# Optimization experiments

Measured on AMD Instinct MI355X. Metric: run time of the kernel, lower is better.

The kernel has to match this reference:

```python
import jax, jax.numpy as jnp
import numpy as np

B, C, H, W = 16, 384, 56, 56
NH, WS, SS = 12, 7, 3          # num_heads, window_size, shift_size
MLP = 4 * C
N = WS * WS                     # tokens per window (49)
nHW = H // WS                   # windows per side (8)
nW = nHW * nHW                  # windows per image (64)
HD = C // NH                    # head dim (32)
EPS = 1e-5


def _ln(x, g, b):
    mu = jnp.mean(x, axis=-1, keepdims=True)
    var = jnp.mean(jnp.square(x - mu), axis=-1, keepdims=True)
    return (x - mu) * jax.lax.rsqrt(var + EPS) * g + b


def _attn_mask():
    # static shifted-window mask, computed once with numpy (constants)
    img = np.zeros((H, W))
    sl = (slice(0, -WS), slice(-WS, -SS), slice(-SS, None))
    cnt = 0
    for hs in sl:
        for ws_ in sl:
            img[hs, ws_] = cnt
            cnt += 1
    mw = img.reshape(nHW, WS, nHW, WS).transpose(0, 2, 1, 3).reshape(-1, N)
    d = mw[:, None, :] - mw[:, :, None]          # (nW, N, N)
    return jnp.asarray(np.where(d != 0, -100.0, 0.0), jnp.float32)

_MASK = _attn_mask()


def setup_inputs() -> dict:
    key = jax.random.key(0)
    ks = jax.random.split(key, 6)
    rn = lambda k, s: jax.random.normal(k, s, jnp.float32) * 0.02
    return {
        "x": jax.random.normal(ks[0], (B, C, H, W), jnp.float32),
        "norm1_g": jnp.ones((C,), jnp.float32),
        "norm1_b": jnp.zeros((C,), jnp.float32),
        "qkv_w": rn(ks[1], (C, 3 * C)),
        "qkv_b": jnp.zeros((3 * C,), jnp.float32),
        "proj_w": rn(ks[2], (C, C)),
        "proj_b": jnp.zeros((C,), jnp.float32),
        "norm2_g": jnp.ones((C,), jnp.float32),
        "norm2_b": jnp.zeros((C,), jnp.float32),
        "fc1_w": rn(ks[3], (C, MLP)),
        "fc1_b": jnp.zeros((MLP,), jnp.float32),
        "fc2_w": rn(ks[4], (MLP, C)),
        "fc2_b": jnp.zeros((C,), jnp.float32),
    }


def reference(x, norm1_g, norm1_b, qkv_w, qkv_b, proj_w, proj_b,
              norm2_g, norm2_b, fc1_w, fc1_b, fc2_w, fc2_b):
    shortcut = x                                   # (B, C, H, W)
    xh = jnp.transpose(x, (0, 2, 3, 1))            # (B, H, W, C)
    xh = _ln(xh, norm1_g, norm1_b)
    # H, W divisible by WS -> padding is a no-op; shifted window path
    xs = jnp.roll(xh, (-SS, -SS), axis=(1, 2))
    # window partition -> (B*nW, N, C)
    xw = xs.reshape(B, nHW, WS, nHW, WS, C).transpose(0, 1, 3, 2, 4, 5)
    xw = xw.reshape(-1, N, C)
    # attention
    qkv = (xw @ qkv_w + qkv_b).reshape(-1, N, 3, NH, HD).transpose(2, 0, 3, 1, 4)
    q, k, v = qkv[0] * HD ** -0.5, qkv[1], qkv[2]  # (B*nW, NH, N, HD)
    attn = jnp.einsum('whnd,whmd->whnm', q, k)     # (B*nW, NH, N, N)
    attn = attn.reshape(B, nW, NH, N, N) + _MASK[None, :, None]
    attn = jax.nn.softmax(attn, axis=-1).reshape(-1, NH, N, N)
    out = jnp.einsum('whnm,whmd->whnd', attn, v)   # (B*nW, NH, N, HD)
    out = out.transpose(0, 2, 1, 3).reshape(-1, N, C)
    out = out @ proj_w + proj_b
    # window reverse -> (B, H, W, C), un-shift
    xs = out.reshape(B, nHW, nHW, WS, WS, C).transpose(0, 1, 3, 2, 4, 5)
    xs = xs.reshape(B, H, W, C)
    xh = jnp.roll(xs, (SS, SS), axis=(1, 2))
    x2 = shortcut + jnp.transpose(xh, (0, 3, 1, 2))
    # MLP residual (in BHWC)
    xh2 = jnp.transpose(x2, (0, 2, 3, 1))
    h = jax.nn.gelu(_ln(xh2, norm2_g, norm2_b) @ fc1_w + fc1_b,
                    approximate=False) @ fc2_w + fc2_b
    xh2 = xh2 + h
    return jnp.transpose(xh2, (0, 3, 1, 2))
```

## Files before the change

kernel.cpp:

```cpp
#include <hip/hip_runtime.h>
#include <hip/hip_bf16.h>
#include <math.h>
#include <stdint.h>

#define C_ 384
#define TOKENS 50176

typedef __bf16 bf16;
typedef __bf16 bf16x8 __attribute__((ext_vector_type(8)));
typedef __bf16 bf16x4 __attribute__((ext_vector_type(4)));
typedef float  f32x4  __attribute__((ext_vector_type(4)));

__device__ __forceinline__ float b2f(bf16 x) { return (float)x; }
__device__ __forceinline__ bf16  f2b(float x) { return (bf16)x; }

__device__ __forceinline__ float fast_gelu(float v) {
    float u2 = v * fmaf(v * v, 0.07135481f, 1.5957691f);
    return v / (1.0f + __expf(-u2));
}

__device__ __forceinline__ void gld_lds16(const bf16* g, bf16* l) {
    __builtin_amdgcn_global_load_lds(
        (const __attribute__((address_space(1))) void*)g,
        (__attribute__((address_space(3))) void*)l, 16, 0, 0);
}

__global__ void wtrans_kernel(const float* __restrict__ in, bf16* __restrict__ out,
                              int K, int N) {
    int idx = blockIdx.x * 256 + threadIdx.x;
    if (idx >= K * N) return;
    int n = idx / K, k = idx % K;
    out[idx] = f2b(in[(size_t)k * N + n]);
}

__global__ __launch_bounds__(256) void ln1_gather_kernel(
    const float* __restrict__ x, const float* __restrict__ g,
    const float* __restrict__ bt, bf16* __restrict__ xw) {
    int wave = threadIdx.x >> 6, lane = threadIdx.x & 63;
    int T = blockIdx.x * 4 + wave;
    int wi = T / 49, n = T % 49;
    int b = wi >> 6, w64 = wi & 63;
    int bh = w64 >> 3, bw = w64 & 7;
    int hs = bh * 7 + n / 7 + 3; if (hs >= 56) hs -= 56;
    int wsd = bw * 7 + n % 7 + 3; if (wsd >= 56) wsd -= 56;
    const float* xp = x + (size_t)b * C_ * 3136 + hs * 56 + wsd;
    float v[6];
    #pragma unroll
    for (int k = 0; k < 6; k++) v[k] = xp[(size_t)(lane + k * 64) * 3136];
    float s = v[0] + v[1] + v[2] + v[3] + v[4] + v[5];
    #pragma unroll
    for (int m = 32; m; m >>= 1) s += __shfl_xor(s, m);
    float mu = s * (1.0f / 384.0f);
    float s2 = 0.f;
    #pragma unroll
    for (int k = 0; k < 6; k++) { float d = v[k] - mu; s2 += d * d; }
    #pragma unroll
    for (int m = 32; m; m >>= 1) s2 += __shfl_xor(s2, m);
    float rstd = rsqrtf(s2 * (1.0f / 384.0f) + 1e-5f);
    bf16* op = xw + (size_t)T * 384;
    #pragma unroll
    for (int k = 0; k < 6; k++) {
        int c = lane + k * 64;
        op[c] = f2b((v[k] - mu) * rstd * g[c] + bt[c]);
    }
}

enum { EPI_NONE = 0, EPI_GELU = 1, EPI_PROJ = 2, EPI_FC2 = 3 };

__device__ __forceinline__ void stage_tile(const bf16* const (&gA)[4], const bf16* const (&gB)[4],
                                           bf16* Asb, bf16* Bsb, int t, int k0) {
    #pragma unroll
    for (int p = 0; p < 4; p++) gld_lds16(gA[p] + k0, Asb + (p * 256 + t) * 8);
    #pragma unroll
    for (int p = 0; p < 4; p++) gld_lds16(gB[p] + k0, Bsb + (p * 256 + t) * 8);
}

__device__ __forceinline__ void compute_tile(const bf16* Asb, const bf16* Bsb,
                                             int aoff0, int aoff1, int boff0, int boff1,
                                             f32x4 (&acc)[4][4]) {
    bf16x8 af[2][4], bfr[2][4];
    __builtin_amdgcn_sched_barrier(0);
    #pragma unroll
    for (int i = 0; i < 4; i++) {
        af[0][i] = *(const bf16x8*)((const char*)Asb + aoff0 + i * 2048);
        af[1][i] = *(const bf16x8*)((const char*)Asb + aoff1 + i * 2048);
    }
    #pragma unroll
    for (int j = 0; j < 4; j++) {
        bfr[0][j] = *(const bf16x8*)((const char*)Bsb + boff0 + j * 2048);
        bfr[1][j] = *(const bf16x8*)((const char*)Bsb + boff1 + j * 2048);
    }
    __builtin_amdgcn_sched_barrier(0);
    __builtin_amdgcn_s_setprio(1);
    #pragma unroll
    for (int kk = 0; kk < 2; kk++)
        #pragma unroll
        for (int j = 0; j < 4; j++)
            #pragma unroll
            for (int i = 0; i < 4; i++)
                acc[j][i] = __builtin_amdgcn_mfma_f32_16x16x32_bf16(bfr[kk][j], af[kk][i], acc[j][i], 0, 0, 0);
    __builtin_amdgcn_s_setprio(0);
    __builtin_amdgcn_sched_barrier(0);
}

#define SYNC_FENCE() do { __builtin_amdgcn_sched_barrier(0); \
                          __builtin_amdgcn_s_barrier(); \
                          __builtin_amdgcn_sched_barrier(0); } while (0)

template <int EPI>
__global__ __launch_bounds__(256, 2) void gemm_kernel(
    const bf16* __restrict__ A, const bf16* __restrict__ Wt,
    const float* __restrict__ bias, bf16* __restrict__ Cout,
    int Kdim, int Ndim,
    const float* __restrict__ resx,
    const bf16* __restrict__ resb) {
    __shared__ __align__(16) bf16 As[2][128 * 64];
    __shared__ __align__(16) bf16 Bs[2][128 * 64];
    int t = threadIdx.x;

    int nwg = gridDim.x * gridDim.y;
    int bid = blockIdx.y * gridDim.x + blockIdx.x;
    int q8 = nwg >> 3, r8 = nwg & 7, xcd = bid & 7, off = bid >> 3;
    int swz = (xcd < r8 ? xcd * (q8 + 1) : r8 * (q8 + 1) + (xcd - r8) * q8) + off;
    int n0 = (swz % gridDim.x) * 128;
    int m0 = (swz / gridDim.x) * 128;

    int lane = t & 63, wave = t >> 6;
    int wr = wave >> 1, wc = wave & 1;
    int quad = lane >> 4, lm = lane & 15;
    f32x4 acc[4][4] = {};

    const bf16* gA[4]; const bf16* gB[4];
    #pragma unroll
    for (int p = 0; p < 4; p++) {
        int idx = p * 256 + t;
        int row = idx >> 3, g = idx & 7;
        int gs = g ^ (row & 7);
        gA[p] = A  + (size_t)(m0 + row) * Kdim + gs * 8;
        gB[p] = Wt + (size_t)(n0 + row) * Kdim + gs * 8;
    }

    int g0 = quad ^ (lm & 7);
    int aoff0 = ((wr * 64 + lm) * 64 + g0 * 8) * 2;
    int boff0 = ((wc * 64 + lm) * 64 + g0 * 8) * 2;
    int aoff1 = aoff0 ^ 64;
    int boff1 = boff0 ^ 64;

    int nt = Kdim >> 6;
    stage_tile(gA, gB, As[0], Bs[0], t, 0);
    stage_tile(gA, gB, As[1], Bs[1], t, 64);
    asm volatile("s_waitcnt vmcnt(8)" ::: "memory");
    SYNC_FENCE();

    for (int tk = 0; tk < nt; tk += 2) {
        compute_tile(As[0], Bs[0], aoff0, aoff1, boff0, boff1, acc);
        SYNC_FENCE();
        if (tk + 2 < nt) {
            stage_tile(gA, gB, As[0], Bs[0], t, (tk + 2) << 6);
            asm volatile("s_waitcnt vmcnt(8)" ::: "memory");
        } else {
            asm volatile("s_waitcnt vmcnt(0)" ::: "memory");
        }
        SYNC_FENCE();
        compute_tile(As[1], Bs[1], aoff0, aoff1, boff0, boff1, acc);
        if (tk + 2 < nt) {
            SYNC_FENCE();
            if (tk + 3 < nt) {
                stage_tile(gA, gB, As[1], Bs[1], t, (tk + 3) << 6);
                asm volatile("s_waitcnt vmcnt(8)" ::: "memory");
            } else {
                asm volatile("s_waitcnt vmcnt(0)" ::: "memory");
            }
            SYNC_FENCE();
        }
    }

    #pragma unroll
    for (int i = 0; i < 4; i++) {
        int m = m0 + wr * 64 + i * 16 + lm;
        size_t resbase = 0;
        if (EPI == EPI_PROJ) {
            int wi = m / 49, n_ = m % 49;
            int b = wi >> 6, w64 = wi & 63;
            int bh = w64 >> 3, bw = w64 & 7;
            int hs = bh * 7 + n_ / 7 + 3; if (hs >= 56) hs -= 56;
            int wsd = bw * 7 + n_ % 7 + 3; if (wsd >= 56) wsd -= 56;
            resbase = (size_t)b * C_ * 3136 + hs * 56 + wsd;
        }
        #pragma unroll
        for (int j = 0; j < 4; j++) {
            int nb = n0 + wc * 64 + j * 16 + quad * 4;
            f32x4 bj = *(const f32x4*)(bias + nb);
            f32x4 v;
            #pragma unroll
            for (int r = 0; r < 4; r++) v[r] = acc[j][i][r] + bj[r];
            if (EPI == EPI_GELU) {
                #pragma unroll
                for (int r = 0; r < 4; r++) v[r] = fast_gelu(v[r]);
            }
            if (EPI == EPI_PROJ) {
                #pragma unroll
                for (int r = 0; r < 4; r++) v[r] += resx[resbase + (size_t)(nb + r) * 3136];
            }
            if (EPI == EPI_FC2) {
                bf16x4 rb = *(const bf16x4*)(resb + (size_t)m * 384 + nb);
                #pragma unroll
                for (int r = 0; r < 4; r++) v[r] += b2f(rb[r]);
            }
            bf16x4 o;
            #pragma unroll
            for (int r = 0; r < 4; r++) o[r] = f2b(v[r]);
            *(bf16x4*)(Cout + (size_t)m * Ndim + nb) = o;
        }
    }
}

__global__ __launch_bounds__(64) void attn_mfma_kernel(const bf16* __restrict__ qkv,
                                                       bf16* __restrict__ aout) {
    __shared__ __align__(16) bf16 pbuf[64 * 72];
    __shared__ int reg_[64];
    int l = threadIdx.x;
    int wi = blockIdx.x / 12, h = blockIdx.x % 12;
    int i16 = l & 15, quad = l >> 4;

    {
        int tok = l < 49 ? l : 48;
        int w64 = wi & 63;
        int bh = w64 >> 3, bw = w64 & 7;
        int hh = bh * 7 + tok / 7, ww = bw * 7 + tok % 7;
        int fh = hh < 49 ? 0 : (hh < 53 ? 1 : 2);
        int fw = ww < 49 ? 0 : (ww < 53 ? 1 : 2);
        reg_[l] = fh * 3 + fw;
    }
    __syncthreads();

    const bf16* qbase = qkv + (size_t)wi * 49 * 1152 + h * 32;

    f32x4 s_[4][4] = {};
    bf16x8 af[4], bfr[4];
    #pragma unroll
    for (int mi = 0; mi < 4; mi++) {
        int m = mi * 16 + i16; if (m > 48) m = 48;
        af[mi] = *(const bf16x8*)(qbase + (size_t)m * 1152 + quad * 8);
    }
    #pragma unroll
    for (int nt = 0; nt < 4; nt++) {
        int n = nt * 16 + i16; if (n > 48) n = 48;
        bfr[nt] = *(const bf16x8*)(qbase + 384 + (size_t)n * 1152 + quad * 8);
    }
    #pragma unroll
    for (int mi = 0; mi < 4; mi++)
        #pragma unroll
        for (int nt = 0; nt < 4; nt++)
            s_[mi][nt] = __builtin_amdgcn_mfma_f32_16x16x32_bf16(af[mi], bfr[nt], s_[mi][nt], 0, 0, 0);

    int creg[4];
    #pragma unroll
    for (int nt = 0; nt < 4; nt++) {
        int c = nt * 16 + i16; if (c > 48) c = 48;
        creg[nt] = reg_[c];
    }

    const float scale = 0.17677669529663687f;
    #pragma unroll
    for (int mi = 0; mi < 4; mi++) {
        #pragma unroll
        for (int r = 0; r < 4; r++) {
            int row = mi * 16 + quad * 4 + r;
            int rreg = reg_[row];
            float v[4]; float mx = -1e30f;
            #pragma unroll
            for (int nt = 0; nt < 4; nt++) {
                int c = nt * 16 + i16;
                float x = s_[mi][nt][r] * scale;
                if (c > 48) x = -1e30f;
                else if (rreg != creg[nt]) x -= 100.0f;
                v[nt] = x; mx = fmaxf(mx, x);
            }
            #pragma unroll
            for (int m = 8; m; m >>= 1) mx = fmaxf(mx, __shfl_xor(mx, m));
            float sum = 0.f;
            #pragma unroll
            for (int nt = 0; nt < 4; nt++) { v[nt] = __expf(v[nt] - mx); sum += v[nt]; }
            #pragma unroll
            for (int m = 8; m; m >>= 1) sum += __shfl_xor(sum, m);
            float inv = 1.0f / sum;
            #pragma unroll
            for (int nt = 0; nt < 4; nt++)
                pbuf[row * 72 + nt * 16 + i16] = f2b(v[nt] * inv);
        }
    }
    __syncthreads();

    f32x4 o_[4][2] = {};
    const bf16* vbase = qkv + (size_t)wi * 49 * 1152 + 768 + h * 32;
    #pragma unroll
    for (int ks = 0; ks < 2; ks++) {
        bf16x8 pa[4];
        #pragma unroll
        for (int mi = 0; mi < 4; mi++)
            pa[mi] = *(const bf16x8*)(pbuf + (mi * 16 + i16) * 72 + ks * 32 + quad * 8);
        bf16x8 vb[2];
        #pragma unroll
        for (int nt = 0; nt < 2; nt++)
            #pragma unroll
            for (int j = 0; j < 8; j++) {
                int tok = ks * 32 + quad * 8 + j; if (tok > 48) tok = 48;
                vb[nt][j] = vbase[(size_t)tok * 1152 + nt * 16 + i16];
            }
        #pragma unroll
        for (int mi = 0; mi < 4; mi++)
            #pragma unroll
            for (int nt = 0; nt < 2; nt++)
                o_[mi][nt] = __builtin_amdgcn_mfma_f32_16x16x32_bf16(pa[mi], vb[nt], o_[mi][nt], 0, 0, 0);
    }

    bf16* obase = aout + (size_t)wi * 49 * 384 + h * 32;
    #pragma unroll
    for (int mi = 0; mi < 4; mi++)
        #pragma unroll
        for (int r = 0; r < 4; r++) {
            int row = mi * 16 + quad * 4 + r;
            if (row < 49) {
                #pragma unroll
                for (int nt = 0; nt < 2; nt++)
                    obase[(size_t)row * 384 + nt * 16 + i16] = f2b(o_[mi][nt][r]);
            }
        }
}

__global__ __launch_bounds__(256) void ln2_kernel(const bf16* __restrict__ x2,
                                                  const float* __restrict__ g,
                                                  const float* __restrict__ bt,
                                                  bf16* __restrict__ x2n) {
    int wave = threadIdx.x >> 6, lane = threadIdx.x & 63;
    int T = blockIdx.x * 4 + wave;
    const bf16* xp = x2 + (size_t)T * 384;
    float v[6];
    #pragma unroll
    for (int k = 0; k < 6; k++) v[k] = b2f(xp[lane + k * 64]);
    float s = v[0] + v[1] + v[2] + v[3] + v[4] + v[5];
    #pragma unroll
    for (int m = 32; m; m >>= 1) s += __shfl_xor(s, m);
    float mu = s * (1.0f / 384.0f);
    float s2 = 0.f;
    #pragma unroll
    for (int k = 0; k < 6; k++) { float d = v[k] - mu; s2 += d * d; }
    #pragma unroll
    for (int m = 32; m; m >>= 1) s2 += __shfl_xor(s2, m);
    float rstd = rsqrtf(s2 * (1.0f / 384.0f) + 1e-5f);
    bf16* op = x2n + (size_t)T * 384;
    #pragma unroll
    for (int k = 0; k < 6; k++) {
        int c = lane + k * 64;
        op[c] = f2b((v[k] - mu) * rstd * g[c] + bt[c]);
    }
}

__global__ __launch_bounds__(256) void untile_kernel(const bf16* __restrict__ otok,
                                                     float* __restrict__ out) {
    __shared__ float tile[56 * 65];
    int t = threadIdx.x;
    int b = blockIdx.x / 336;
    int rem = blockIdx.x % 336;
    int h = rem / 6;
    int c0 = (rem % 6) * 64;
    int hs = h + 53; if (hs >= 56) hs -= 56;
    int bh = hs / 7, th = hs % 7;
    #pragma unroll
    for (int pass = 0; pass < 14; pass++) {
        int w = pass * 4 + (t >> 6);
        int c = t & 63;
        int wsd = w + 53; if (wsd >= 56) wsd -= 56;
        int T = (b * 64 + bh * 8 + wsd / 7) * 49 + th * 7 + wsd % 7;
        tile[w * 65 + c] = b2f(otok[(size_t)T * 384 + c0 + c]);
    }
    __syncthreads();
    #pragma unroll
    for (int pass = 0; pass < 14; pass++) {
        int idx = pass * 256 + t;
        int c = idx / 56, w = idx % 56;
        out[((size_t)(b * 384 + c0 + c)) * 3136 + h * 56 + w] = tile[w * 65 + c];
    }
}

extern "C" void kernel_launch(void* const* d_in, const int* in_sizes, int n_in,
                              void* d_out, int out_size, void* d_ws, size_t ws_size,
                              hipStream_t stream) {
    (void)in_sizes; (void)n_in; (void)out_size; (void)ws_size;
    const float* x      = (const float*)d_in[0];
    const float* n1g    = (const float*)d_in[1];
    const float* n1b    = (const float*)d_in[2];
    const float* qkv_w  = (const float*)d_in[3];
    const float* qkv_b  = (const float*)d_in[4];
    const float* proj_w = (const float*)d_in[5];
    const float* proj_b = (const float*)d_in[6];
    const float* n2g    = (const float*)d_in[7];
    const float* n2b    = (const float*)d_in[8];
    const float* fc1_w  = (const float*)d_in[9];
    const float* fc1_b  = (const float*)d_in[10];
    const float* fc2_w  = (const float*)d_in[11];
    const float* fc2_b  = (const float*)d_in[12];
    float* out = (float*)d_out;
    char* ws = (char*)d_ws;

    bf16* qkv_wT = (bf16*)(ws + 0);
    bf16* proj_wT = (bf16*)(ws + 884736);
    bf16* fc1_wT = (bf16*)(ws + 1179648);
    bf16* fc2_wT = (bf16*)(ws + 2359296);
    bf16* xw   = (bf16*)(ws + 4194304);
    bf16* qkvb = (bf16*)(ws + 42729472);
    bf16* attn = (bf16*)(ws + 158334976);
    bf16* x2   = (bf16*)(ws + 4194304);
    bf16* x2n  = (bf16*)(ws + 42729472);
    bf16* h1   = (bf16*)(ws + 81264640);
    bf16* otok = (bf16*)(ws + 235405312);

    wtrans_kernel<<<(384 * 1152 + 255) / 256, 256, 0, stream>>>(qkv_w, qkv_wT, 384, 1152);
    wtrans_kernel<<<(384 * 384 + 255) / 256, 256, 0, stream>>>(proj_w, proj_wT, 384, 384);
    wtrans_kernel<<<(384 * 1536 + 255) / 256, 256, 0, stream>>>(fc1_w, fc1_wT, 384, 1536);
    wtrans_kernel<<<(1536 * 384 + 255) / 256, 256, 0, stream>>>(fc2_w, fc2_wT, 1536, 384);

    ln1_gather_kernel<<<TOKENS / 4, 256, 0, stream>>>(x, n1g, n1b, xw);

    gemm_kernel<EPI_NONE><<<dim3(9, 392), 256, 0, stream>>>(
        xw, qkv_wT, qkv_b, qkvb, 384, 1152, nullptr, nullptr);

    attn_mfma_kernel<<<12288, 64, 0, stream>>>(qkvb, attn);

    gemm_kernel<EPI_PROJ><<<dim3(3, 392), 256, 0, stream>>>(
        attn, proj_wT, proj_b, x2, 384, 384, x, nullptr);

    ln2_kernel<<<TOKENS / 4, 256, 0, stream>>>(x2, n2g, n2b, x2n);

    gemm_kernel<EPI_GELU><<<dim3(12, 392), 256, 0, stream>>>(
        x2n, fc1_wT, fc1_b, h1, 384, 1536, nullptr, nullptr);

    gemm_kernel<EPI_FC2><<<dim3(3, 392), 256, 0, stream>>>(
        h1, fc2_wT, fc2_b, otok, 1536, 384, nullptr, x2);

    untile_kernel<<<16 * 336, 256, 0, stream>>>(otok, out);
}
```

Baseline: 654.0 us.

## Add persistent weight-stationary GEMM for K=384 layers with streamed A tiles

Adds a persistent 512-thread GEMM kernel that loads a full 128x384 weight panel into LDS once. It then streams 256-row A tiles through a double buffer, with epilogues fused per tile, across 252 workgroups. The qkv, proj and fc1 GEMMs use this kernel, while fc2 keeps the old kernel because its K is 1536. The goal is to stop reloading weight tiles for every output tile and to save launch/tail overhead, at the cost of one workgroup per CU and large LDS use.

```diff
diff --git a/kernel.cpp b/kernel.cpp
--- a/kernel.cpp
+++ b/kernel.cpp
@@ -5,6 +5,7 @@
 
 #define C_ 384
 #define TOKENS 50176
+#define MTILES 196
 
 typedef __bf16 bf16;
 typedef __bf16 bf16x8 __attribute__((ext_vector_type(8)));
@@ -24,6 +25,10 @@
         (const __attribute__((address_space(1))) void*)g,
         (__attribute__((address_space(3))) void*)l, 16, 0, 0);
 }
+
+#define SYNC_FENCE() do { __builtin_amdgcn_sched_barrier(0); \
+                          __builtin_amdgcn_s_barrier(); \
+                          __builtin_amdgcn_sched_barrier(0); } while (0)
 
 __global__ void wtrans_kernel(const float* __restrict__ in, bf16* __restrict__ out,
                               int K, int N) {
@@ -67,17 +72,160 @@
 
 enum { EPI_NONE = 0, EPI_GELU = 1, EPI_PROJ = 2, EPI_FC2 = 3 };
 
-__device__ __forceinline__ void stage_tile(const bf16* const (&gA)[4], const bf16* const (&gB)[4],
-                                           bf16* Asb, bf16* Bsb, int t, int k0) {
+
+__device__ __forceinline__ void stage_A(const bf16* const (&gAs)[4], bf16* dst,
+                                        int t, int koff) {
+    #pragma unroll
+    for (int p = 0; p < 4; p++) gld_lds16(gAs[p] + koff, dst + (p * 512 + t) * 8);
+}
+
+__device__ __forceinline__ void compute_step(const bf16* Asb, const bf16* Wsb,
+                                             int abase, int wbase, int tkb,
+                                             f32x4 (&acc)[4][4]) {
+    bf16x8 af[2][4], bw[2][4];
+    __builtin_amdgcn_sched_barrier(0);
+    #pragma unroll
+    for (int i = 0; i < 4; i++) {
+        af[0][i] = *(const bf16x8*)((const char*)Asb + abase + i * 2048);
+        af[1][i] = *(const bf16x8*)((const char*)Asb + (abase ^ 64) + i * 2048);
+    }
+    #pragma unroll
+    for (int j = 0; j < 4; j++) {
+        bw[0][j] = *(const bf16x8*)((const char*)Wsb + wbase + tkb + j * 12288);
+        bw[1][j] = *(const bf16x8*)((const char*)Wsb + (wbase ^ 64) + tkb + j * 12288);
+    }
+    __builtin_amdgcn_sched_barrier(0);
+    __builtin_amdgcn_s_setprio(1);
+    #pragma unroll
+    for (int kk = 0; kk < 2; kk++)
+        #pragma unroll
+        for (int j = 0; j < 4; j++)
+            #pragma unroll
+            for (int i = 0; i < 4; i++)
+                acc[j][i] = __builtin_amdgcn_mfma_f32_16x16x32_bf16(bw[kk][j], af[kk][i], acc[j][i], 0, 0, 0);
+    __builtin_amdgcn_s_setprio(0);
+    __builtin_amdgcn_sched_barrier(0);
+}
+
+template <int EPI>
+__global__ __launch_bounds__(512, 1) void gemm_wp_kernel(
+    const bf16* __restrict__ A, const bf16* __restrict__ Wt,
+    const float* __restrict__ bias, bf16* __restrict__ Cout,
+    int Ndim, int NPANEL, int PPN,
+    const float* __restrict__ resx) {
+    __shared__ __align__(16) bf16 As[2][256 * 64];
+    __shared__ __align__(16) bf16 Ws[128 * 384];
+    int t = threadIdx.x;
+    int panel = blockIdx.x % NPANEL, pb = blockIdx.x / NPANEL;
+    int n0 = panel * 128;
+    int lo = (MTILES * pb) / PPN, hi = (MTILES * (pb + 1)) / PPN;
+    int ntile = hi - lo;
+
+    #pragma unroll
+    for (int q = 0; q < 12; q++) {
+        int idx = q * 512 + t;
+        int row = idx / 48, cg = idx % 48;
+        int sg = (cg & ~7) | ((cg & 7) ^ (row & 7));
+        gld_lds16(Wt + (size_t)(n0 + row) * 384 + sg * 8, &Ws[0] + idx * 8);
+    }
+    const bf16* gAs[4];
+    #pragma unroll
+    for (int q = 0; q < 4; q++) {
+        int idx = q * 512 + t;
+        int row = idx >> 3, g = idx & 7;
+        int gs = g ^ (row & 7);
+        gAs[q] = A + (size_t)(lo * 256 + row) * 384 + gs * 8;
+    }
+    stage_A(gAs, As[0], t, 0);
+    stage_A(gAs, As[1], t, 64);
+    int sk = 2;
+    int remaining = ntile * 6 - 2;
+    asm volatile("s_waitcnt vmcnt(4)" ::: "memory");
+    SYNC_FENCE();
+
+    int lane = t & 63, wave = t >> 6;
+    int wr = wave >> 1, wc = wave & 1;
+    int quad = lane >> 4, lm = lane & 15;
+    int g0b = (quad ^ (lm & 7)) * 16;
+    int abase = (wr * 64 + lm) * 128 + g0b;
+    int wbase = (wc * 64 + lm) * 768 + g0b;
+    f32x4 acc[4][4] = {};
+
+    int par = 0;
+    for (int lmt = 0; lmt < ntile; ++lmt) {
+        #pragma unroll
+        for (int tk = 0; tk < 6; ++tk) {
+            compute_step(As[par], Ws, abase, wbase, tk * 128, acc);
+            if (tk == 5) {
+                int m0e = (lo + lmt) * 256;
+                #pragma unroll
+                for (int i = 0; i < 4; i++) {
+                    int m = m0e + wr * 64 + i * 16 + lm;
+                    size_t resbase = 0;
+                    if (EPI == EPI_PROJ) {
+                        int wi = m / 49, n_ = m % 49;
+                        int b = wi >> 6, w64 = wi & 63;
+                        int bh = w64 >> 3, bw = w64 & 7;
+                        int hs = bh * 7 + n_ / 7 + 3; if (hs >= 56) hs -= 56;
+                        int wsd = bw * 7 + n_ % 7 + 3; if (wsd >= 56) wsd -= 56;
+                        resbase = (size_t)b * C_ * 3136 + hs * 56 + wsd;
+                    }
+                    #pragma unroll
+                    for (int j = 0; j < 4; j++) {
+                        int nb = n0 + wc * 64 + j * 16 + quad * 4;
+                        f32x4 bj = *(const f32x4*)(bias + nb);
+                        f32x4 v;
+                        #pragma unroll
+                        for (int r = 0; r < 4; r++) v[r] = acc[j][i][r] + bj[r];
+                        if (EPI == EPI_GELU) {
+                            #pragma unroll
+                            for (int r = 0; r < 4; r++) v[r] = fast_gelu(v[r]);
+                        }
+                        if (EPI == EPI_PROJ) {
+                            #pragma unroll
+                            for (int r = 0; r < 4; r++) v[r] += resx[resbase + (size_t)(nb + r) * 3136];
+                        }
+                        bf16x4 o;
+                        #pragma unroll
+                        for (int r = 0; r < 4; r++) o[r] = f2b(v[r]);
+                        *(bf16x4*)(Cout + (size_t)m * Ndim + nb) = o;
+                        #pragma unroll
+                        for (int r = 0; r < 4; r++) acc[j][i][r] = 0.f;
+                    }
+                }
+            }
+            SYNC_FENCE();
+            if (remaining > 0) {
+                stage_A(gAs, As[par], t, sk * 64);
+                remaining--;
+                if (++sk == 6) {
+                    sk = 0;
+                    #pragma unroll
+                    for (int q = 0; q < 4; q++) gAs[q] += 256 * 384;
+                }
+                if (tk == 5) asm volatile("s_waitcnt vmcnt(20)" ::: "memory");
+                else         asm volatile("s_waitcnt vmcnt(4)"  ::: "memory");
+            } else {
+                if (tk == 5) asm volatile("s_waitcnt vmcnt(16)" ::: "memory");
+                else         asm volatile("s_waitcnt vmcnt(0)"  ::: "memory");
+            }
+            SYNC_FENCE();
+            par ^= 1;
+        }
+    }
+}
+
+__device__ __forceinline__ void stage_tile4(const bf16* const (&gA)[4], const bf16* const (&gB)[4],
+                                            bf16* Asb, bf16* Bsb, int t, int k0) {
     #pragma unroll
     for (int p = 0; p < 4; p++) gld_lds16(gA[p] + k0, Asb + (p * 256 + t) * 8);
     #pragma unroll
     for (int p = 0; p < 4; p++) gld_lds16(gB[p] + k0, Bsb + (p * 256 + t) * 8);
 }
 
-__device__ __forceinline__ void compute_tile(const bf16* Asb, const bf16* Bsb,
-                                             int aoff0, int aoff1, int boff0, int boff1,
-                                             f32x4 (&acc)[4][4]) {
+__device__ __forceinline__ void compute_tile4(const bf16* Asb, const bf16* Bsb,
+                                              int aoff0, int aoff1, int boff0, int boff1,
+                                              f32x4 (&acc)[4][4]) {
     bf16x8 af[2][4], bfr[2][4];
     __builtin_amdgcn_sched_barrier(0);
     #pragma unroll
@@ -102,10 +250,6 @@
     __builtin_amdgcn_s_setprio(0);
     __builtin_amdgcn_sched_barrier(0);
 }
-
-#define SYNC_FENCE() do { __builtin_amdgcn_sched_barrier(0); \
-                          __builtin_amdgcn_s_barrier(); \
-                          __builtin_amdgcn_sched_barrier(0); } while (0)
 
 template <int EPI>
 __global__ __launch_bounds__(256, 2) void gemm_kernel(
@@ -147,26 +291,26 @@
     int boff1 = boff0 ^ 64;
 
     int nt = Kdim >> 6;
-    stage_tile(gA, gB, As[0], Bs[0], t, 0);
-    stage_tile(gA, gB, As[1], Bs[1], t, 64);
+    stage_tile4(gA, gB, As[0], Bs[0], t, 0);
+    stage_tile4(gA, gB, As[1], Bs[1], t, 64);
     asm volatile("s_waitcnt vmcnt(8)" ::: "memory");
     SYNC_FENCE();
 
     for (int tk = 0; tk < nt; tk += 2) {
-        compute_tile(As[0], Bs[0], aoff0, aoff1, boff0, boff1, acc);
+        compute_tile4(As[0], Bs[0], aoff0, aoff1, boff0, boff1, acc);
         SYNC_FENCE();
         if (tk + 2 < nt) {
-            stage_tile(gA, gB, As[0], Bs[0], t, (tk + 2) << 6);
+            stage_tile4(gA, gB, As[0], Bs[0], t, (tk + 2) << 6);
             asm volatile("s_waitcnt vmcnt(8)" ::: "memory");
         } else {
             asm volatile("s_waitcnt vmcnt(0)" ::: "memory");
         }
         SYNC_FENCE();
-        compute_tile(As[1], Bs[1], aoff0, aoff1, boff0, boff1, acc);
+        compute_tile4(As[1], Bs[1], aoff0, aoff1, boff0, boff1, acc);
         if (tk + 2 < nt) {
             SYNC_FENCE();
             if (tk + 3 < nt) {
-                stage_tile(gA, gB, As[1], Bs[1], t, (tk + 3) << 6);
+                stage_tile4(gA, gB, As[1], Bs[1], t, (tk + 3) << 6);
                 asm volatile("s_waitcnt vmcnt(8)" ::: "memory");
             } else {
                 asm volatile("s_waitcnt vmcnt(0)" ::: "memory");
@@ -178,15 +322,6 @@
     #pragma unroll
     for (int i = 0; i < 4; i++) {
         int m = m0 + wr * 64 + i * 16 + lm;
-        size_t resbase = 0;
-        if (EPI == EPI_PROJ) {
-            int wi = m / 49, n_ = m % 49;
-            int b = wi >> 6, w64 = wi & 63;
-            int bh = w64 >> 3, bw = w64 & 7;
-            int hs = bh * 7 + n_ / 7 + 3; if (hs >= 56) hs -= 56;
-            int wsd = bw * 7 + n_ % 7 + 3; if (wsd >= 56) wsd -= 56;
-            resbase = (size_t)b * C_ * 3136 + hs * 56 + wsd;
-        }
         #pragma unroll
         for (int j = 0; j < 4; j++) {
             int nb = n0 + wc * 64 + j * 16 + quad * 4;
@@ -197,10 +332,6 @@
             if (EPI == EPI_GELU) {
                 #pragma unroll
                 for (int r = 0; r < 4; r++) v[r] = fast_gelu(v[r]);
-            }
-            if (EPI == EPI_PROJ) {
-                #pragma unroll
-                for (int r = 0; r < 4; r++) v[r] += resx[resbase + (size_t)(nb + r) * 3136];
             }
             if (EPI == EPI_FC2) {
                 bf16x4 rb = *(const bf16x4*)(resb + (size_t)m * 384 + nb);
@@ -423,18 +554,18 @@
 
     ln1_gather_kernel<<<TOKENS / 4, 256, 0, stream>>>(x, n1g, n1b, xw);
 
-    gemm_kernel<EPI_NONE><<<dim3(9, 392), 256, 0, stream>>>(
-        xw, qkv_wT, qkv_b, qkvb, 384, 1152, nullptr, nullptr);
+    gemm_wp_kernel<EPI_NONE><<<252, 512, 0, stream>>>(
+        xw, qkv_wT, qkv_b, qkvb, 1152, 9, 28, nullptr);
 
     attn_mfma_kernel<<<12288, 64, 0, stream>>>(qkvb, attn);
 
-    gemm_kernel<EPI_PROJ><<<dim3(3, 392), 256, 0, stream>>>(
-        attn, proj_wT, proj_b, x2, 384, 384, x, nullptr);
+    gemm_wp_kernel<EPI_PROJ><<<252, 512, 0, stream>>>(
+        attn, proj_wT, proj_b, x2, 384, 3, 84, x);
 
     ln2_kernel<<<TOKENS / 4, 256, 0, stream>>>(x2, n2g, n2b, x2n);
 
-    gemm_kernel<EPI_GELU><<<dim3(12, 392), 256, 0, stream>>>(
-        x2n, fc1_wT, fc1_b, h1, 384, 1536, nullptr, nullptr);
+    gemm_wp_kernel<EPI_GELU><<<252, 512, 0, stream>>>(
+        x2n, fc1_wT, fc1_b, h1, 1536, 12, 21, nullptr);
 
     gemm_kernel<EPI_FC2><<<dim3(3, 392), 256, 0, stream>>>(
         h1, fc2_wT, fc2_b, otok, 1536, 384, nullptr, x2);
```

New measurement: 714.8 us. 9.3% more time.

## Enlarge GEMM tiles to 512x128 with 8 waves and interleaved LDS/MFMA

Applied to the files above, without the earlier changes.

The shared GEMM kernel moves from 128x128 tiles with 4 waves to 512x128 tiles with 8 waves. Each wave now computes a 128x64 sub-tile, which raises arithmetic intensity and cuts the number of B-tile reloads. The compute step is split into four MFMA groups, with the LDS loads for the next group issued between them and paced by explicit lgkmcnt waits. The cost is larger LDS use (160KB double-buffered), one block per CU, more accumulator registers, and fewer blocks in the grid, which could hurt occupancy and tail balance.

```diff
diff --git a/kernel.cpp b/kernel.cpp
--- a/kernel.cpp
+++ b/kernel.cpp
@@ -24,6 +24,10 @@
         (const __attribute__((address_space(1))) void*)g,
         (__attribute__((address_space(3))) void*)l, 16, 0, 0);
 }
+
+#define SYNC_FENCE() do { __builtin_amdgcn_sched_barrier(0); \
+                          __builtin_amdgcn_s_barrier(); \
+                          __builtin_amdgcn_sched_barrier(0); } while (0)
 
 __global__ void wtrans_kernel(const float* __restrict__ in, bf16* __restrict__ out,
                               int K, int N) {
@@ -67,54 +71,68 @@
 
 enum { EPI_NONE = 0, EPI_GELU = 1, EPI_PROJ = 2, EPI_FC2 = 3 };
 
-__device__ __forceinline__ void stage_tile(const bf16* const (&gA)[4], const bf16* const (&gB)[4],
+
+__device__ __forceinline__ void stage_tile(const bf16* const (&gA)[8], const bf16* const (&gB)[2],
                                            bf16* Asb, bf16* Bsb, int t, int k0) {
     #pragma unroll
-    for (int p = 0; p < 4; p++) gld_lds16(gA[p] + k0, Asb + (p * 256 + t) * 8);
-    #pragma unroll
-    for (int p = 0; p < 4; p++) gld_lds16(gB[p] + k0, Bsb + (p * 256 + t) * 8);
-}
-
-__device__ __forceinline__ void compute_tile(const bf16* Asb, const bf16* Bsb,
-                                             int aoff0, int aoff1, int boff0, int boff1,
-                                             f32x4 (&acc)[4][4]) {
-    bf16x8 af[2][4], bfr[2][4];
+    for (int p = 0; p < 8; p++) gld_lds16(gA[p] + k0, Asb + (p * 512 + t) * 8);
+    #pragma unroll
+    for (int p = 0; p < 2; p++) gld_lds16(gB[p] + k0, Bsb + (p * 512 + t) * 8);
+}
+
+#define MFMA16(ACC, BQ, AQ, IB)                                                   \
+    do {                                                                          \
+        __builtin_amdgcn_s_setprio(1);                                            \
+        _Pragma("unroll")                                                         \
+        for (int j_ = 0; j_ < 4; j_++)                                            \
+            _Pragma("unroll")                                                     \
+            for (int i_ = 0; i_ < 4; i_++)                                        \
+                ACC[(IB) + i_][j_] = __builtin_amdgcn_mfma_f32_16x16x32_bf16(     \
+                    BQ[j_], AQ[i_], ACC[(IB) + i_][j_], 0, 0, 0);                 \
+        __builtin_amdgcn_s_setprio(0);                                            \
+        __builtin_amdgcn_sched_barrier(0);                                        \
+    } while (0)
+
+__device__ __forceinline__ void compute_step(const bf16* Asb, const bf16* Bsb,
+                                             int aB, int bB, f32x4 (&acc)[8][4]) {
+    const char* Ab = (const char*)Asb;
+    const char* Bb = (const char*)Bsb;
+    bf16x8 a0[4], a1[4], b0[4], b1[4];
     __builtin_amdgcn_sched_barrier(0);
     #pragma unroll
-    for (int i = 0; i < 4; i++) {
-        af[0][i] = *(const bf16x8*)((const char*)Asb + aoff0 + i * 2048);
-        af[1][i] = *(const bf16x8*)((const char*)Asb + aoff1 + i * 2048);
-    }
-    #pragma unroll
-    for (int j = 0; j < 4; j++) {
-        bfr[0][j] = *(const bf16x8*)((const char*)Bsb + boff0 + j * 2048);
-        bfr[1][j] = *(const bf16x8*)((const char*)Bsb + boff1 + j * 2048);
-    }
+    for (int i = 0; i < 4; i++) a0[i] = *(const bf16x8*)(Ab + aB + i * 2048);
+    #pragma unroll
+    for (int j = 0; j < 4; j++) b0[j] = *(const bf16x8*)(Bb + bB + j * 2048);
+    #pragma unroll
+    for (int i = 0; i < 4; i++) a1[i] = *(const bf16x8*)(Ab + aB + (i + 4) * 2048);
+    asm volatile("s_waitcnt lgkmcnt(4)" ::: "memory");
     __builtin_amdgcn_sched_barrier(0);
-    __builtin_amdgcn_s_setprio(1);
-    #pragma unroll
-    for (int kk = 0; kk < 2; kk++)
-        #pragma unroll
-        for (int j = 0; j < 4; j++)
-            #pragma unroll
-            for (int i = 0; i < 4; i++)
-                acc[j][i] = __builtin_amdgcn_mfma_f32_16x16x32_bf16(bfr[kk][j], af[kk][i], acc[j][i], 0, 0, 0);
-    __builtin_amdgcn_s_setprio(0);
+    MFMA16(acc, b0, a0, 0);
+    #pragma unroll
+    for (int i = 0; i < 4; i++) a0[i] = *(const bf16x8*)(Ab + (aB ^ 64) + i * 2048);
+    #pragma unroll
+    for (int j = 0; j < 4; j++) b1[j] = *(const bf16x8*)(Bb + (bB ^ 64) + j * 2048);
+    asm volatile("s_waitcnt lgkmcnt(8)" ::: "memory");
     __builtin_amdgcn_sched_barrier(0);
-}
-
-#define SYNC_FENCE() do { __builtin_amdgcn_sched_barrier(0); \
-                          __builtin_amdgcn_s_barrier(); \
-                          __builtin_amdgcn_sched_barrier(0); } while (0)
+    MFMA16(acc, b0, a1, 4);
+    #pragma unroll
+    for (int i = 0; i < 4; i++) a1[i] = *(const bf16x8*)(Ab + (aB ^ 64) + (i + 4) * 2048);
+    asm volatile("s_waitcnt lgkmcnt(4)" ::: "memory");
+    __builtin_amdgcn_sched_barrier(0);
+    MFMA16(acc, b1, a0, 0);
+    asm volatile("s_waitcnt lgkmcnt(0)" ::: "memory");
+    __builtin_amdgcn_sched_barrier(0);
+    MFMA16(acc, b1, a1, 4);
+}
 
 template <int EPI>
-__global__ __launch_bounds__(256, 2) void gemm_kernel(
+__global__ __launch_bounds__(512, 1) void gemm_kernel(
     const bf16* __restrict__ A, const bf16* __restrict__ Wt,
     const float* __restrict__ bias, bf16* __restrict__ Cout,
     int Kdim, int Ndim,
     const float* __restrict__ resx,
     const bf16* __restrict__ resb) {
-    __shared__ __align__(16) bf16 As[2][128 * 64];
+    __shared__ __align__(16) bf16 As[2][512 * 64];
     __shared__ __align__(16) bf16 Bs[2][128 * 64];
     int t = threadIdx.x;
 
@@ -123,51 +141,47 @@
     int q8 = nwg >> 3, r8 = nwg & 7, xcd = bid & 7, off = bid >> 3;
     int swz = (xcd < r8 ? xcd * (q8 + 1) : r8 * (q8 + 1) + (xcd - r8) * q8) + off;
     int n0 = (swz % gridDim.x) * 128;
-    int m0 = (swz / gridDim.x) * 128;
+    int m0 = (swz / gridDim.x) * 512;
 
     int lane = t & 63, wave = t >> 6;
     int wr = wave >> 1, wc = wave & 1;
     int quad = lane >> 4, lm = lane & 15;
-    f32x4 acc[4][4] = {};
-
-    const bf16* gA[4]; const bf16* gB[4];
-    #pragma unroll
-    for (int p = 0; p < 4; p++) {
-        int idx = p * 256 + t;
+    f32x4 acc[8][4] = {};
+
+    const bf16* gA[8]; const bf16* gB[2];
+    #pragma unroll
+    for (int p = 0; p < 8; p++) {
+        int idx = p * 512 + t;
         int row = idx >> 3, g = idx & 7;
         int gs = g ^ (row & 7);
-        gA[p] = A  + (size_t)(m0 + row) * Kdim + gs * 8;
+        gA[p] = A + (size_t)(m0 + row) * Kdim + gs * 8;
+    }
+    #pragma unroll
+    for (int p = 0; p < 2; p++) {
+        int idx = p * 512 + t;
+        int row = idx >> 3, g = idx & 7;
+        int gs = g ^ (row & 7);
         gB[p] = Wt + (size_t)(n0 + row) * Kdim + gs * 8;
     }
 
-    int g0 = quad ^ (lm & 7);
-    int aoff0 = ((wr * 64 + lm) * 64 + g0 * 8) * 2;
-    int boff0 = ((wc * 64 + lm) * 64 + g0 * 8) * 2;
-    int aoff1 = aoff0 ^ 64;
-    int boff1 = boff0 ^ 64;
+    int g0b = (quad ^ (lm & 7)) * 16;
+    int aB = (wr * 128 + lm) * 128 + g0b;
+    int bB = (wc * 64 + lm) * 128 + g0b;
 
     int nt = Kdim >> 6;
     stage_tile(gA, gB, As[0], Bs[0], t, 0);
     stage_tile(gA, gB, As[1], Bs[1], t, 64);
-    asm volatile("s_waitcnt vmcnt(8)" ::: "memory");
+    asm volatile("s_waitcnt vmcnt(10)" ::: "memory");
     SYNC_FENCE();
 
-    for (int tk = 0; tk < nt; tk += 2) {
-        compute_tile(As[0], Bs[0], aoff0, aoff1, boff0, boff1, acc);
-        SYNC_FENCE();
-        if (tk + 2 < nt) {
-            stage_tile(gA, gB, As[0], Bs[0], t, (tk + 2) << 6);
-            asm volatile("s_waitcnt vmcnt(8)" ::: "memory");
-        } else {
-            asm volatile("s_waitcnt vmcnt(0)" ::: "memory");
-        }
-        SYNC_FENCE();
-        compute_tile(As[1], Bs[1], aoff0, aoff1, boff0, boff1, acc);
-        if (tk + 2 < nt) {
+    for (int tk = 0; tk < nt; ++tk) {
+        int par = tk & 1;
+        compute_step(As[par], Bs[par], aB, bB, acc);
+        if (tk + 1 < nt) {
             SYNC_FENCE();
-            if (tk + 3 < nt) {
-                stage_tile(gA, gB, As[1], Bs[1], t, (tk + 3) << 6);
-                asm volatile("s_waitcnt vmcnt(8)" ::: "memory");
+            if (tk + 2 < nt) {
+                stage_tile(gA, gB, As[par], Bs[par], t, (tk + 2) << 6);
+                asm volatile("s_waitcnt vmcnt(10)" ::: "memory");
             } else {
                 asm volatile("s_waitcnt vmcnt(0)" ::: "memory");
             }
@@ -176,8 +190,8 @@
     }
 
     #pragma unroll
-    for (int i = 0; i < 4; i++) {
-        int m = m0 + wr * 64 + i * 16 + lm;
+    for (int i = 0; i < 8; i++) {
+        int m = m0 + wr * 128 + i * 16 + lm;
         size_t resbase = 0;
         if (EPI == EPI_PROJ) {
             int wi = m / 49, n_ = m % 49;
@@ -193,7 +207,7 @@
             f32x4 bj = *(const f32x4*)(bias + nb);
             f32x4 v;
             #pragma unroll
-            for (int r = 0; r < 4; r++) v[r] = acc[j][i][r] + bj[r];
+            for (int r = 0; r < 4; r++) v[r] = acc[i][j][r] + bj[r];
             if (EPI == EPI_GELU) {
                 #pragma unroll
                 for (int r = 0; r < 4; r++) v[r] = fast_gelu(v[r]);
@@ -423,20 +437,20 @@
 
     ln1_gather_kernel<<<TOKENS / 4, 256, 0, stream>>>(x, n1g, n1b, xw);
 
-    gemm_kernel<EPI_NONE><<<dim3(9, 392), 256, 0, stream>>>(
+    gemm_kernel<EPI_NONE><<<dim3(9, 98), 512, 0, stream>>>(
         xw, qkv_wT, qkv_b, qkvb, 384, 1152, nullptr, nullptr);
 
     attn_mfma_kernel<<<12288, 64, 0, stream>>>(qkvb, attn);
 
-    gemm_kernel<EPI_PROJ><<<dim3(3, 392), 256, 0, stream>>>(
+    gemm_kernel<EPI_PROJ><<<dim3(3, 98), 512, 0, stream>>>(
         attn, proj_wT, proj_b, x2, 384, 384, x, nullptr);
 
     ln2_kernel<<<TOKENS / 4, 256, 0, stream>>>(x2, n2g, n2b, x2n);
 
-    gemm_kernel<EPI_GELU><<<dim3(12, 392), 256, 0, stream>>>(
+    gemm_kernel<EPI_GELU><<<dim3(12, 98), 512, 0, stream>>>(
         x2n, fc1_wT, fc1_b, h1, 384, 1536, nullptr, nullptr);
 
-    gemm_kernel<EPI_FC2><<<dim3(3, 392), 256, 0, stream>>>(
+    gemm_kernel<EPI_FC2><<<dim3(3, 98), 512, 0, stream>>>(
         h1, fc2_wT, fc2_b, otok, 1536, 384, nullptr, x2);
 
     untile_kernel<<<16 * 336, 256, 0, stream>>>(otok, out);
```

Result: slower. 761.9 us (+16.5%).

## Load GEMM A operand directly from global into registers, bypassing LDS

Applied to the files above, without the earlier changes.

The GEMM kernel no longer stages the A tile in shared memory. Each wave loads its A fragments straight from global memory into registers with inline global_load_dwordx4, double-buffered across even and odd k-tiles, while B is still staged through LDS with async global-to-LDS loads. This halves LDS traffic and shared memory per block, which could allow more occupancy. In exchange, global accesses per thread are less coalesced, register pressure rises from the A prefetch buffers, and the hand-counted vmcnt waits must stay exactly right.

```diff
diff --git a/kernel.cpp b/kernel.cpp
--- a/kernel.cpp
+++ b/kernel.cpp
@@ -24,6 +24,13 @@
         (const __attribute__((address_space(1))) void*)g,
         (__attribute__((address_space(3))) void*)l, 16, 0, 0);
 }
+
+#define SB() __builtin_amdgcn_sched_barrier(0)
+#define SYNC_FENCE() do { __builtin_amdgcn_sched_barrier(0); \
+                          __builtin_amdgcn_s_barrier(); \
+                          __builtin_amdgcn_sched_barrier(0); } while (0)
+#define WAITVM(N) do { asm volatile("s_waitcnt vmcnt(" #N ")" ::: "memory"); SB(); } while (0)
+#define WAITLG()  do { asm volatile("s_waitcnt lgkmcnt(0)" ::: "memory"); SB(); } while (0)
 
 __global__ void wtrans_kernel(const float* __restrict__ in, bf16* __restrict__ out,
                               int K, int N) {
@@ -67,45 +74,58 @@
 
 enum { EPI_NONE = 0, EPI_GELU = 1, EPI_PROJ = 2, EPI_FC2 = 3 };
 
-__device__ __forceinline__ void stage_tile(const bf16* const (&gA)[4], const bf16* const (&gB)[4],
-                                           bf16* Asb, bf16* Bsb, int t, int k0) {
-    #pragma unroll
-    for (int p = 0; p < 4; p++) gld_lds16(gA[p] + k0, Asb + (p * 256 + t) * 8);
+
+__device__ __forceinline__ void ldg_a2(f32x4& d0, f32x4& d1, const bf16* p) {
+    asm volatile("global_load_dwordx4 %0, %2, off\n\t"
+                 "global_load_dwordx4 %1, %2, off offset:64"
+                 : "=&v"(d0), "=&v"(d1) : "v"(p) : "memory");
+}
+
+__device__ __forceinline__ void stage_B(const bf16* const (&gB)[4], bf16* Bsb,
+                                        int t, int k0) {
     #pragma unroll
     for (int p = 0; p < 4; p++) gld_lds16(gB[p] + k0, Bsb + (p * 256 + t) * 8);
 }
 
-__device__ __forceinline__ void compute_tile(const bf16* Asb, const bf16* Bsb,
-                                             int aoff0, int aoff1, int boff0, int boff1,
-                                             f32x4 (&acc)[4][4]) {
-    bf16x8 af[2][4], bfr[2][4];
-    __builtin_amdgcn_sched_barrier(0);
-    #pragma unroll
-    for (int i = 0; i < 4; i++) {
-        af[0][i] = *(const bf16x8*)((const char*)Asb + aoff0 + i * 2048);
-        af[1][i] = *(const bf16x8*)((const char*)Asb + aoff1 + i * 2048);
-    }
-    #pragma unroll
-    for (int j = 0; j < 4; j++) {
-        bfr[0][j] = *(const bf16x8*)((const char*)Bsb + boff0 + j * 2048);
-        bfr[1][j] = *(const bf16x8*)((const char*)Bsb + boff1 + j * 2048);
-    }
-    __builtin_amdgcn_sched_barrier(0);
-    __builtin_amdgcn_s_setprio(1);
-    #pragma unroll
-    for (int kk = 0; kk < 2; kk++)
-        #pragma unroll
-        for (int j = 0; j < 4; j++)
-            #pragma unroll
-            for (int i = 0; i < 4; i++)
-                acc[j][i] = __builtin_amdgcn_mfma_f32_16x16x32_bf16(bfr[kk][j], af[kk][i], acc[j][i], 0, 0, 0);
-    __builtin_amdgcn_s_setprio(0);
-    __builtin_amdgcn_sched_barrier(0);
-}
-
-#define SYNC_FENCE() do { __builtin_amdgcn_sched_barrier(0); \
-                          __builtin_amdgcn_s_barrier(); \
-                          __builtin_amdgcn_sched_barrier(0); } while (0)
+#define LDA(A0, A1)                                                     \
+    do {                                                                \
+        _Pragma("unroll")                                               \
+        for (int i_ = 0; i_ < 4; i_++) ldg_a2(A0[i_], A1[i_], ga[i_]);  \
+        _Pragma("unroll")                                               \
+        for (int i_ = 0; i_ < 4; i_++) ga[i_] += 64;                    \
+    } while (0)
+
+#define RDB(Bsb)                                                              \
+    do {                                                                      \
+        const char* Bb_ = (const char*)(Bsb);                                 \
+        _Pragma("unroll")                                                     \
+        for (int j_ = 0; j_ < 4; j_++)                                        \
+            b0[j_] = *(const bf16x8*)(Bb_ + bB + j_ * 2048);                  \
+        _Pragma("unroll")                                                     \
+        for (int j_ = 0; j_ < 4; j_++)                                        \
+            b1[j_] = *(const bf16x8*)(Bb_ + (bB ^ 64) + j_ * 2048);           \
+    } while (0)
+
+#define MMAC(A0, A1)                                                           \
+    do {                                                                       \
+        __builtin_amdgcn_s_setprio(1);                                         \
+        _Pragma("unroll")                                                      \
+        for (int j_ = 0; j_ < 4; j_++)                                         \
+            _Pragma("unroll")                                                  \
+            for (int i_ = 0; i_ < 4; i_++)                                     \
+                acc[j_][i_] = __builtin_amdgcn_mfma_f32_16x16x32_bf16(         \
+                    b0[j_], __builtin_bit_cast(bf16x8, A0[i_]), acc[j_][i_],   \
+                    0, 0, 0);                                                  \
+        _Pragma("unroll")                                                      \
+        for (int j_ = 0; j_ < 4; j_++)                                         \
+            _Pragma("unroll")                                                  \
+            for (int i_ = 0; i_ < 4; i_++)                                     \
+                acc[j_][i_] = __builtin_amdgcn_mfma_f32_16x16x32_bf16(         \
+                    b1[j_], __builtin_bit_cast(bf16x8, A1[i_]), acc[j_][i_],   \
+                    0, 0, 0);                                                  \
+        __builtin_amdgcn_s_setprio(0);                                         \
+        __builtin_amdgcn_sched_barrier(0);                                     \
+    } while (0)
 
 template <int EPI>
 __global__ __launch_bounds__(256, 2) void gemm_kernel(
@@ -114,7 +134,6 @@
     int Kdim, int Ndim,
     const float* __restrict__ resx,
     const bf16* __restrict__ resb) {
-    __shared__ __align__(16) bf16 As[2][128 * 64];
     __shared__ __align__(16) bf16 Bs[2][128 * 64];
     int t = threadIdx.x;
 
@@ -130,47 +149,59 @@
     int quad = lane >> 4, lm = lane & 15;
     f32x4 acc[4][4] = {};
 
-    const bf16* gA[4]; const bf16* gB[4];
+    const bf16* gB[4];
     #pragma unroll
     for (int p = 0; p < 4; p++) {
         int idx = p * 256 + t;
         int row = idx >> 3, g = idx & 7;
         int gs = g ^ (row & 7);
-        gA[p] = A  + (size_t)(m0 + row) * Kdim + gs * 8;
         gB[p] = Wt + (size_t)(n0 + row) * Kdim + gs * 8;
     }
-
     int g0 = quad ^ (lm & 7);
-    int aoff0 = ((wr * 64 + lm) * 64 + g0 * 8) * 2;
-    int boff0 = ((wc * 64 + lm) * 64 + g0 * 8) * 2;
-    int aoff1 = aoff0 ^ 64;
-    int boff1 = boff0 ^ 64;
+    int bB = ((wc * 64 + lm) * 64 + g0 * 8) * 2;
+
+    const bf16* ga[4];
+    #pragma unroll
+    for (int i = 0; i < 4; i++)
+        ga[i] = A + (size_t)(m0 + wr * 64 + i * 16 + lm) * Kdim + quad * 8;
+
+    f32x4 aE0[4], aE1[4], aO0[4], aO1[4];
+    bf16x8 b0[4], b1[4];
 
     int nt = Kdim >> 6;
-    stage_tile(gA, gB, As[0], Bs[0], t, 0);
-    stage_tile(gA, gB, As[1], Bs[1], t, 64);
-    asm volatile("s_waitcnt vmcnt(8)" ::: "memory");
+    stage_B(gB, Bs[0], t, 0);
+    stage_B(gB, Bs[1], t, 64);
+    LDA(aE0, aE1);
+    WAITVM(0);
     SYNC_FENCE();
 
     for (int tk = 0; tk < nt; tk += 2) {
-        compute_tile(As[0], Bs[0], aoff0, aoff1, boff0, boff1, acc);
+        RDB(Bs[0]);
+        LDA(aO0, aO1);
+        WAITVM(12);
+        WAITLG();
+        MMAC(aE0, aE1);
         SYNC_FENCE();
         if (tk + 2 < nt) {
-            stage_tile(gA, gB, As[0], Bs[0], t, (tk + 2) << 6);
-            asm volatile("s_waitcnt vmcnt(8)" ::: "memory");
+            stage_B(gB, Bs[0], t, (tk + 2) << 6);
+            WAITVM(12);
         } else {
-            asm volatile("s_waitcnt vmcnt(0)" ::: "memory");
+            WAITVM(8);
         }
         SYNC_FENCE();
-        compute_tile(As[1], Bs[1], aoff0, aoff1, boff0, boff1, acc);
+        RDB(Bs[1]);
+        if (tk + 2 < nt) {
+            LDA(aE0, aE1);
+            WAITVM(12);
+        } else {
+            WAITVM(0);
+        }
+        WAITLG();
+        MMAC(aO0, aO1);
         if (tk + 2 < nt) {
             SYNC_FENCE();
-            if (tk + 3 < nt) {
-                stage_tile(gA, gB, As[1], Bs[1], t, (tk + 3) << 6);
-                asm volatile("s_waitcnt vmcnt(8)" ::: "memory");
-            } else {
-                asm volatile("s_waitcnt vmcnt(0)" ::: "memory");
-            }
+            stage_B(gB, Bs[1], t, (tk + 3) << 6);
+            WAITVM(12);
             SYNC_FENCE();
         }
     }
```

Measured after the change: 794.6 us. +21.5%, slower.
